# Optimization experiments

Measured on AMD Instinct MI355X. Metric: run time of the kernel, lower is better.

The kernel has to match this reference:

```python
import jax, jax.numpy as jnp
import numpy as np

N, D, OUT, E, K = 65536, 256, 256, 8, 2  # tokens, input_dim, output_dim, num_experts, top-k


def setup_inputs() -> dict:
    key = jax.random.key(0)
    k1, k2, k3, k4 = jax.random.split(key, 4)
    x = jax.random.normal(k1, (N, D), dtype=jnp.float32)
    # xavier_normal-like init for the gate
    w_gate = jax.random.normal(k2, (D, E), dtype=jnp.float32) * np.float32(np.sqrt(2.0 / (D + E)))
    # PWLayer params stacked over experts: bias init zeros, weight std 0.02
    expert_bias = jax.random.normal(k3, (E, D), dtype=jnp.float32) * 0.01
    expert_weight = jax.random.normal(k4, (E, OUT, D), dtype=jnp.float32) * 0.02
    return {"x": x, "w_gate": w_gate, "expert_bias": expert_bias, "expert_weight": expert_weight}


def reference(x, w_gate, expert_bias, expert_weight):
    # --- noisy_top_k_gating (eval mode: clean logits only) ---
    logits = x @ w_gate                                   # [N, E]
    top_v, top_i = jax.lax.top_k(logits, K)               # [N, K]
    sparse_logits = jnp.full_like(logits, -jnp.inf)
    rows = jnp.arange(logits.shape[0])[:, None]           # [N, 1]
    sparse_logits = sparse_logits.at[rows, top_i].set(top_v)
    gates = jax.nn.softmax(sparse_logits, axis=-1)        # [N, E], zeros off the top-k
    # --- dense all-expert PWLayer pass: (x - bias_e) @ W_e^T ---
    centered = x[:, None, :] - expert_bias[None, :, :]    # [N, E, D]
    expert_stack = jnp.einsum('ned,eod->neo', centered, expert_weight)  # [N, E, OUT]
    # --- gated combine ---
    return jnp.einsum('ne,neo->no', gates, expert_stack)  # [N, OUT]
```

## Files before the change

### kernel.cpp

```cpp
#include <hip/hip_runtime.h>
#include <hip/hip_bf16.h>
#include <math.h>

#define N_TOK 65536
#define DIM   256
#define NEXP  8

using frag_ab = __attribute__((ext_vector_type(8))) short;
using frag_cd = __attribute__((ext_vector_type(4))) float;

__device__ __forceinline__ unsigned short f2bf(float f) {
  unsigned u = __float_as_uint(f);
  u += 0x7FFFu + ((u >> 16) & 1u);
  return (unsigned short)(u >> 16);
}

__device__ __forceinline__ void gl2lds16(const unsigned short* g, unsigned short* l) {
  __builtin_amdgcn_global_load_lds(
      (const __attribute__((address_space(1))) void*)g,
      (__attribute__((address_space(3))) void*)l, 16, 0, 0);
}


__global__ __launch_bounds__(256) void k_prep(
    const float* __restrict__ w,
    const float* __restrict__ bias,
    unsigned short* __restrict__ Wb,
    float* __restrict__ c,
    int* __restrict__ meta) {
  int tid = threadIdx.x;
  int wid = (blockIdx.x * 256 + tid) >> 6;
  int lane = tid & 63;
  int e = wid >> 8, o = wid & 255;
  const float* wr = w + (size_t)(e * 256 + o) * DIM + lane * 4;
  float4 wv = *(const float4*)wr;
  const float* br = bias + e * DIM + lane * 4;
  float4 bv = *(const float4*)br;
  float s = wv.x * bv.x + wv.y * bv.y + wv.z * bv.z + wv.w * bv.w;
  #pragma unroll
  for (int m = 1; m < 64; m <<= 1) s += __shfl_xor(s, m, 64);
  if (lane == 0) c[e * 256 + o] = s;
  ushort4 h; h.x = f2bf(wv.x); h.y = f2bf(wv.y); h.z = f2bf(wv.z); h.w = f2bf(wv.w);
  *(ushort4*)(Wb + (size_t)e * 65536 + (size_t)(lane >> 1) * 2048 + o * 8 + (lane & 1) * 4) = h;
  if (blockIdx.x == 0 && tid < 192) meta[tid] = 0;
}

__global__ __launch_bounds__(256) void k_gating(
    const float* __restrict__ x,
    const float* __restrict__ wg,
    unsigned short* __restrict__ xb,
    int* __restrict__ routeE,
    float* __restrict__ routeG,
    int* __restrict__ meta) {
  __shared__ double swg[DIM * NEXP];
  __shared__ float  chunk[64 * 35];
  __shared__ int    hcnt[64];
  int tid = threadIdx.x;
  int tok0 = blockIdx.x * 64;
  int tk = tid >> 2, sub = tid & 3;

  for (int i = tid; i < DIM * NEXP; i += 256) swg[i] = (double)wg[i];
  if (tid < 64) hcnt[tid] = 0;

  double p[NEXP];
  #pragma unroll
  for (int e = 0; e < NEXP; e++) p[e] = 0.0;

  int f0 = tid, f1 = 256 + tid;
  int r0 = f0 >> 3, c40 = (f0 & 7) * 4;
  int r1 = f1 >> 3, c41 = (f1 & 7) * 4;
  const float* xs0 = x + (size_t)(tok0 + r0) * DIM + c40;
  const float* xs1 = x + (size_t)(tok0 + r1) * DIM + c41;
  unsigned short* xd0 = xb + (size_t)(tok0 + r0) * DIM + c40;
  unsigned short* xd1 = xb + (size_t)(tok0 + r1) * DIM + c41;

  float4 v0 = *(const float4*)(xs0);
  float4 v1 = *(const float4*)(xs1);

  for (int dc = 0; dc < 8; dc++) {
    __syncthreads();
    {
      ushort4 h0; h0.x = f2bf(v0.x); h0.y = f2bf(v0.y); h0.z = f2bf(v0.z); h0.w = f2bf(v0.w);
      ushort4 h1; h1.x = f2bf(v1.x); h1.y = f2bf(v1.y); h1.z = f2bf(v1.z); h1.w = f2bf(v1.w);
      *(ushort4*)(xd0 + dc * 32) = h0;
      *(ushort4*)(xd1 + dc * 32) = h1;
      float* d0 = &chunk[r0 * 35 + c40];
      d0[0] = v0.x; d0[1] = v0.y; d0[2] = v0.z; d0[3] = v0.w;
      float* d1 = &chunk[r1 * 35 + c41];
      d1[0] = v1.x; d1[1] = v1.y; d1[2] = v1.z; d1[3] = v1.w;
    }
    float4 n0 = make_float4(0.f, 0.f, 0.f, 0.f);
    float4 n1 = make_float4(0.f, 0.f, 0.f, 0.f);
    if (dc < 7) {
      n0 = *(const float4*)(xs0 + (dc + 1) * 32);
      n1 = *(const float4*)(xs1 + (dc + 1) * 32);
    }
    __syncthreads();
    #pragma unroll
    for (int c8 = 0; c8 < 8; c8++) {
      int cc = c8 * 4 + sub;
      double xv = (double)chunk[tk * 35 + cc];
      const double* wrow = &swg[(dc * 32 + cc) * NEXP];
      #pragma unroll
      for (int e = 0; e < NEXP; e++) p[e] += xv * wrow[e];
    }
    v0 = n0; v1 = n1;
  }

  #pragma unroll
  for (int e = 0; e < NEXP; e++) {
    p[e] += __shfl_xor(p[e], 1, 64);
    p[e] += __shfl_xor(p[e], 2, 64);
  }

  if (sub == 0) {
    int i1 = 0; double v1d = p[0];
    #pragma unroll
    for (int e = 1; e < NEXP; e++) { if (p[e] > v1d) { v1d = p[e]; i1 = e; } }
    int i2 = -1; double v2d = -1e300;
    #pragma unroll
    for (int e = 0; e < NEXP; e++) { if (e != i1 && p[e] > v2d) { v2d = p[e]; i2 = e; } }
    double t = exp(v2d - v1d);
    float g1 = (float)(1.0 / (1.0 + t));
    float g2 = 1.0f - g1;

    int n = tok0 + tk;
    routeE[n] = i1 | (i2 << 8);
    *(float2*)(routeG + 2 * (size_t)n) = make_float2(g1, g2);
    int a = i1 < i2 ? i1 : i2, b = i1 < i2 ? i2 : i1;
    atomicAdd(&hcnt[a * 8 + b], 1);
  }
  __syncthreads();
  if (tid < 64) atomicAdd(&meta[tid], hcnt[tid]);
}

__global__ void k_scan(int* __restrict__ meta) {
  if (threadIdx.x == 0) {
    int run = 0;
    for (int p = 0; p < 64; p++) {
      meta[64 + p] = run; meta[128 + p] = run;
      run += ((meta[p] + 127) >> 7) << 7;
    }
  }
}

__global__ __launch_bounds__(1024) void k_scatter(
    const int* __restrict__ routeE, const float* __restrict__ routeG,
    int* __restrict__ meta,
    int* __restrict__ srcTok, float* __restrict__ srcGA, float* __restrict__ srcGB) {
  __shared__ int cnt[64], bse[64];
  int tid = threadIdx.x;
  if (tid < 64) cnt[tid] = 0;
  __syncthreads();
  int n = blockIdx.x * 1024 + tid;
  int ep = routeE[n];
  int e1 = ep & 255, e2 = ep >> 8;
  float2 g = *(const float2*)(routeG + 2 * (size_t)n);
  int a = e1 < e2 ? e1 : e2, b = e1 < e2 ? e2 : e1;
  float ga = e1 < e2 ? g.x : g.y;
  float gb = e1 < e2 ? g.y : g.x;
  int pid = a * 8 + b;
  int r = atomicAdd(&cnt[pid], 1);
  __syncthreads();
  if (tid < 64) bse[tid] = atomicAdd(&meta[128 + tid], cnt[tid]);
  __syncthreads();
  int p = bse[pid] + r;
  srcTok[p] = n; srcGA[p] = ga; srcGB[p] = gb;
}

__global__ __launch_bounds__(512, 2) void k_gemm_pair(
    const unsigned short* __restrict__ xb,
    const unsigned short* __restrict__ Wb,
    const int* __restrict__ meta,
    const int* __restrict__ srcTok,
    const float* __restrict__ srcGA, const float* __restrict__ srcGB,
    const float* __restrict__ c,
    float* __restrict__ out) {
  __shared__ unsigned short sA[4][128 * 64];
  __shared__ int   sTok[128];
  __shared__ float sGAs[128], sGBs[128];
  __shared__ float sCorA[256], sCorB[256];
  int tid = threadIdx.x;

  int rem = blockIdx.x, pid = 0, ne = 0;
  for (pid = 0; pid < 64; pid++) {
    ne = meta[pid];
    int tiles = (ne + 127) >> 7;
    if (rem < tiles) break;
    rem -= tiles;
  }
  if (pid == 64) return;
  int ea = pid >> 3, eb = pid & 7;
  int mt = rem;
  int slot0 = meta[64 + pid] + mt * 128;

  if (tid < 128) {
    int idx = mt * 128 + tid;
    bool v = idx < ne;
    sTok[tid]  = v ? srcTok[slot0 + tid] : 0;
    sGAs[tid]  = v ? srcGA[slot0 + tid] : 0.f;
    sGBs[tid]  = v ? srcGB[slot0 + tid] : 1.f;
  } else if (tid < 192) {
    ((float4*)sCorA)[tid - 128] = ((const float4*)(c + ea * 256))[tid - 128];
  } else if (tid < 256) {
    ((float4*)sCorB)[tid - 192] = ((const float4*)(c + eb * 256))[tid - 192];
  }
  __syncthreads();

  int w = tid >> 6, lane = tid & 63;
  int lrow = lane >> 3, lchk = lane & 7;

  #pragma unroll
  for (int q = 0; q < 2; q++) {
    int r0 = w * 16 + q * 8;
    int r  = r0 + lrow;
    int cc = (lchk - r) & 7;
    const unsigned short* src = xb + (size_t)sTok[r] * 256 + cc * 8;
    #pragma unroll
    for (int kk = 0; kk < 4; kk++)
      gl2lds16(src + kk * 64, &sA[kk][r0 * 64]);
  }
  __syncthreads();

  int wm = w & 1, wn = w >> 1;
  int lr = lane & 15, lk = lane >> 4;
  int offA[2][4];
  #pragma unroll
  for (int ks = 0; ks < 2; ks++)
    #pragma unroll
    for (int i = 0; i < 4; i++) {
      int ra = wm * 64 + i * 16 + lr;
      offA[ks][i] = ra * 64 + ((ks * 4 + lk + ra) & 7) * 8;
    }

  const unsigned short* bBaseA =
      Wb + (size_t)ea * 65536 + (size_t)lk * 2048 + (wn * 64 + lr) * 8;
  const unsigned short* bBaseB =
      Wb + (size_t)eb * 65536 + (size_t)lk * 2048 + (wn * 64 + lr) * 8;

  frag_cd acc[4][4];
  #pragma unroll
  for (int i = 0; i < 4; i++)
    #pragma unroll
    for (int j = 0; j < 4; j++)
      acc[i][j] = (frag_cd){0.f, 0.f, 0.f, 0.f};

#define PHASE(BB) do {                                                      \
    _Pragma("unroll")                                                       \
    for (int kk = 0; kk < 4; kk++) {                                        \
      _Pragma("unroll")                                                     \
      for (int ks = 0; ks < 2; ks++) {                                      \
        frag_ab av[4], bv[4];                                               \
        _Pragma("unroll")                                                   \
        for (int j = 0; j < 4; j++)                                         \
          bv[j] = *(const frag_ab*)((BB) + kk * 16384 + ks * 8192 + j * 128); \
        _Pragma("unroll")                                                   \
        for (int i = 0; i < 4; i++) av[i] = *(const frag_ab*)(&sA[kk][0] + offA[ks][i]); \
        _Pragma("unroll")                                                   \
        for (int i = 0; i < 4; i++)                                         \
          _Pragma("unroll")                                                 \
          for (int j = 0; j < 4; j++)                                       \
            acc[i][j] = __builtin_amdgcn_mfma_f32_16x16x32_bf16(av[i], bv[j], acc[i][j], 0, 0, 0); \
      }                                                                     \
    }                                                                       \
  } while (0)

  PHASE(bBaseA);

  #pragma unroll
  for (int i = 0; i < 4; i++)
    #pragma unroll
    for (int rr = 0; rr < 4; rr++) {
      int m = wm * 64 + i * 16 + lk * 4 + rr;
      float ratio = sGAs[m] / sGBs[m];
      #pragma unroll
      for (int j = 0; j < 4; j++) acc[i][j][rr] *= ratio;
    }

  PHASE(bBaseB);

#undef PHASE

  #pragma unroll
  for (int i = 0; i < 4; i++) {
    #pragma unroll
    for (int rr = 0; rr < 4; rr++) {
      int m = wm * 64 + i * 16 + lk * 4 + rr;
      if (mt * 128 + m < ne) {
        int tokn = sTok[m];
        float sa = sGAs[m], sb = sGBs[m];
        float* orow = out + (size_t)tokn * 256;
        #pragma unroll
        for (int j = 0; j < 4; j++) {
          int col = wn * 64 + j * 16 + lr;
          orow[col] = sb * acc[i][j][rr] - (sa * sCorA[col] + sb * sCorB[col]);
        }
      }
    }
  }
}

extern "C" void kernel_launch(void* const* d_in, const int* in_sizes, int n_in,
                              void* d_out, int out_size, void* d_ws, size_t ws_size,
                              hipStream_t stream) {
  const float* x    = (const float*)d_in[0];
  const float* wg   = (const float*)d_in[1];
  const float* bias = (const float*)d_in[2];
  const float* w    = (const float*)d_in[3];
  float* out = (float*)d_out;
  char* ws = (char*)d_ws;

  unsigned short* xb = (unsigned short*)(ws);
  unsigned short* Wb = (unsigned short*)(ws + 33554432);
  float* c           = (float*)(ws + 34603008);
  int* meta          = (int*)(ws + 34611200);
  int* routeE        = (int*)(ws + 34612224);
  float* routeG      = (float*)(ws + 34874368);
  int* srcTok        = (int*)(ws + 35398656);
  float* srcGA       = (float*)(ws + 35678720);
  float* srcGB       = (float*)(ws + 35958784);

  hipLaunchKernelGGL(k_prep,      dim3(512),  dim3(256),  0, stream, w, bias, Wb, c, meta);
  hipLaunchKernelGGL(k_gating,    dim3(1024), dim3(256),  0, stream, x, wg, xb, routeE, routeG, meta);
  hipLaunchKernelGGL(k_scan,      dim3(1),    dim3(64),   0, stream, meta);
  hipLaunchKernelGGL(k_scatter,   dim3(64),   dim3(1024), 0, stream, routeE, routeG, meta,
                     srcTok, srcGA, srcGB);
  hipLaunchKernelGGL(k_gemm_pair, dim3(544),  dim3(512),  0, stream, xb, Wb,
                     meta, srcTok, srcGA, srcGB, c, out);
}
```

Measured before the change: 180.4 us.

## Halve pair-GEMM M tile to 64 rows and double-buffer B fragment loads

Each pair-GEMM block now covers 64 tokens instead of 128, and padding in the scan and the grid size are adjusted to match (1056 blocks). This halves the accumulator registers and the LDS footprint, so launch bounds can ask for 4 blocks per CU. The two expert phases are merged into one 16-step loop that prefetches the next B fragments from global memory while the current MFMAs run. In exchange, each W fragment is reused over fewer rows, which adds global and L2 traffic for W, and the padding overhead per tile changes.

```diff
diff --git a/kernel.cpp b/kernel.cpp
--- a/kernel.cpp
+++ b/kernel.cpp
@@ -139,7 +139,7 @@
     int run = 0;
     for (int p = 0; p < 64; p++) {
       meta[64 + p] = run; meta[128 + p] = run;
-      run += ((meta[p] + 127) >> 7) << 7;
+      run += ((meta[p] + 63) >> 6) << 6;
     }
   }
 }
@@ -168,7 +168,7 @@
   srcTok[p] = n; srcGA[p] = ga; srcGB[p] = gb;
 }
 
-__global__ __launch_bounds__(512, 2) void k_gemm_pair(
+__global__ __launch_bounds__(512, 4) void k_gemm_pair(
     const unsigned short* __restrict__ xb,
     const unsigned short* __restrict__ Wb,
     const int* __restrict__ meta,
@@ -176,33 +176,33 @@
     const float* __restrict__ srcGA, const float* __restrict__ srcGB,
     const float* __restrict__ c,
     float* __restrict__ out) {
-  __shared__ unsigned short sA[4][128 * 64];
-  __shared__ int   sTok[128];
-  __shared__ float sGAs[128], sGBs[128];
+  __shared__ unsigned short sA[4][64 * 64];
+  __shared__ int   sTok[64];
+  __shared__ float sGAs[64], sGBs[64];
   __shared__ float sCorA[256], sCorB[256];
   int tid = threadIdx.x;
 
   int rem = blockIdx.x, pid = 0, ne = 0;
   for (pid = 0; pid < 64; pid++) {
     ne = meta[pid];
-    int tiles = (ne + 127) >> 7;
+    int tiles = (ne + 63) >> 6;
     if (rem < tiles) break;
     rem -= tiles;
   }
   if (pid == 64) return;
   int ea = pid >> 3, eb = pid & 7;
   int mt = rem;
-  int slot0 = meta[64 + pid] + mt * 128;
-
-  if (tid < 128) {
-    int idx = mt * 128 + tid;
+  int slot0 = meta[64 + pid] + mt * 64;
+
+  if (tid < 64) {
+    int idx = mt * 64 + tid;
     bool v = idx < ne;
     sTok[tid]  = v ? srcTok[slot0 + tid] : 0;
     sGAs[tid]  = v ? srcGA[slot0 + tid] : 0.f;
     sGBs[tid]  = v ? srcGB[slot0 + tid] : 1.f;
-  } else if (tid < 192) {
+  } else if (tid >= 128 && tid < 192) {
     ((float4*)sCorA)[tid - 128] = ((const float4*)(c + ea * 256))[tid - 128];
-  } else if (tid < 256) {
+  } else if (tid >= 192 && tid < 256) {
     ((float4*)sCorB)[tid - 192] = ((const float4*)(c + eb * 256))[tid - 192];
   }
   __syncthreads();
@@ -210,26 +210,24 @@
   int w = tid >> 6, lane = tid & 63;
   int lrow = lane >> 3, lchk = lane & 7;
 
-  #pragma unroll
-  for (int q = 0; q < 2; q++) {
-    int r0 = w * 16 + q * 8;
-    int r  = r0 + lrow;
+  {
+    int r = w * 8 + lrow;
     int cc = (lchk - r) & 7;
     const unsigned short* src = xb + (size_t)sTok[r] * 256 + cc * 8;
     #pragma unroll
     for (int kk = 0; kk < 4; kk++)
-      gl2lds16(src + kk * 64, &sA[kk][r0 * 64]);
+      gl2lds16(src + kk * 64, &sA[kk][w * 8 * 64]);
   }
   __syncthreads();
 
   int wm = w & 1, wn = w >> 1;
   int lr = lane & 15, lk = lane >> 4;
-  int offA[2][4];
+  int offA[2][2];
   #pragma unroll
   for (int ks = 0; ks < 2; ks++)
     #pragma unroll
-    for (int i = 0; i < 4; i++) {
-      int ra = wm * 64 + i * 16 + lr;
+    for (int i = 0; i < 2; i++) {
+      int ra = wm * 32 + i * 16 + lr;
       offA[ks][i] = ra * 64 + ((ks * 4 + lk + ra) & 7) * 8;
     }
 
@@ -238,55 +236,57 @@
   const unsigned short* bBaseB =
       Wb + (size_t)eb * 65536 + (size_t)lk * 2048 + (wn * 64 + lr) * 8;
 
-  frag_cd acc[4][4];
-  #pragma unroll
-  for (int i = 0; i < 4; i++)
+  frag_cd acc[2][4];
+  #pragma unroll
+  for (int i = 0; i < 2; i++)
     #pragma unroll
     for (int j = 0; j < 4; j++)
       acc[i][j] = (frag_cd){0.f, 0.f, 0.f, 0.f};
 
-#define PHASE(BB) do {                                                      \
+#define BPTR(C) (((C) < 8 ? bBaseA : bBaseB) + (((C) & 7) >> 1) * 16384 + ((C) & 1) * 8192)
+#define LOADB(DST, C) do {                                                  \
     _Pragma("unroll")                                                       \
-    for (int kk = 0; kk < 4; kk++) {                                        \
-      _Pragma("unroll")                                                     \
-      for (int ks = 0; ks < 2; ks++) {                                      \
-        frag_ab av[4], bv[4];                                               \
-        _Pragma("unroll")                                                   \
-        for (int j = 0; j < 4; j++)                                         \
-          bv[j] = *(const frag_ab*)((BB) + kk * 16384 + ks * 8192 + j * 128); \
-        _Pragma("unroll")                                                   \
-        for (int i = 0; i < 4; i++) av[i] = *(const frag_ab*)(&sA[kk][0] + offA[ks][i]); \
-        _Pragma("unroll")                                                   \
-        for (int i = 0; i < 4; i++)                                         \
-          _Pragma("unroll")                                                 \
-          for (int j = 0; j < 4; j++)                                       \
-            acc[i][j] = __builtin_amdgcn_mfma_f32_16x16x32_bf16(av[i], bv[j], acc[i][j], 0, 0, 0); \
-      }                                                                     \
-    }                                                                       \
+    for (int j = 0; j < 4; j++) DST[j] = *(const frag_ab*)(BPTR(C) + j * 128); \
   } while (0)
 
-  PHASE(bBaseA);
-
-  #pragma unroll
-  for (int i = 0; i < 4; i++)
+  frag_ab bv0[4], bv1[4];
+  LOADB(bv0, 0);
+  #pragma unroll
+  for (int cc = 0; cc < 16; cc++) {
+    frag_ab* cur = (cc & 1) ? bv1 : bv0;
+    frag_ab* nxt = (cc & 1) ? bv0 : bv1;
+    if (cc < 15) LOADB(nxt, cc + 1);
+    if (cc == 8) {
+      #pragma unroll
+      for (int i = 0; i < 2; i++)
+        #pragma unroll
+        for (int rr = 0; rr < 4; rr++) {
+          int m = wm * 32 + i * 16 + lk * 4 + rr;
+          float ratio = sGAs[m] / sGBs[m];
+          #pragma unroll
+          for (int j = 0; j < 4; j++) acc[i][j][rr] *= ratio;
+        }
+    }
+    int ks = cc & 1, kk = (cc & 7) >> 1;
+    frag_ab av[2];
+    #pragma unroll
+    for (int i = 0; i < 2; i++) av[i] = *(const frag_ab*)(&sA[kk][0] + offA[ks][i]);
+    #pragma unroll
+    for (int i = 0; i < 2; i++)
+      #pragma unroll
+      for (int j = 0; j < 4; j++)
+        acc[i][j] = __builtin_amdgcn_mfma_f32_16x16x32_bf16(av[i], cur[j], acc[i][j], 0, 0, 0);
+  }
+
+#undef LOADB
+#undef BPTR
+
+  #pragma unroll
+  for (int i = 0; i < 2; i++) {
     #pragma unroll
     for (int rr = 0; rr < 4; rr++) {
-      int m = wm * 64 + i * 16 + lk * 4 + rr;
-      float ratio = sGAs[m] / sGBs[m];
-      #pragma unroll
-      for (int j = 0; j < 4; j++) acc[i][j][rr] *= ratio;
-    }
-
-  PHASE(bBaseB);
-
-#undef PHASE
-
-  #pragma unroll
-  for (int i = 0; i < 4; i++) {
-    #pragma unroll
-    for (int rr = 0; rr < 4; rr++) {
-      int m = wm * 64 + i * 16 + lk * 4 + rr;
-      if (mt * 128 + m < ne) {
+      int m = wm * 32 + i * 16 + lk * 4 + rr;
+      if (mt * 64 + m < ne) {
         int tokn = sTok[m];
         float sa = sGAs[m], sb = sGBs[m];
         float* orow = out + (size_t)tokn * 256;
@@ -325,6 +325,6 @@
   hipLaunchKernelGGL(k_scan,      dim3(1),    dim3(64),   0, stream, meta);
   hipLaunchKernelGGL(k_scatter,   dim3(64),   dim3(1024), 0, stream, routeE, routeG, meta,
                      srcTok, srcGA, srcGB);
-  hipLaunchKernelGGL(k_gemm_pair, dim3(544),  dim3(512),  0, stream, xb, Wb,
+  hipLaunchKernelGGL(k_gemm_pair, dim3(1056), dim3(512),  0, stream, xb, Wb,
                      meta, srcTok, srcGA, srcGB, c, out);
 }
```

Result: slower. 188.4 us (+4.4%).
